# Kernel tuning notes

Hardware: AMD Instinct MI355X
Metric: run time of the kernel (lower is better)

The kernel has to match this reference:

```python
import jax, jax.numpy as jnp
import numpy as np
from jax import lax

# dims: B=2, C=dim=64, H=W=128 -> N=16384 tokens; d_inner=128, d_state=16, dt_rank=4, d_conv=4

def setup_inputs() -> dict:
    key = jax.random.key(0)
    ks = jax.random.split(key, 8)
    def n(k, shp, scale=0.02):
        return jax.random.normal(k, shp, jnp.float32) * scale
    d_inner, d_state, dt_rank = 128, 16, 4
    return {
        "x": jax.random.normal(ks[0], (2, 64, 128, 128), jnp.float32),
        "ln_w": jnp.ones((64,), jnp.float32),
        "ln_b": jnp.zeros((64,), jnp.float32),
        "in_proj_w": n(ks[1], (2 * d_inner, 64)),
        "conv_w": n(ks[2], (d_inner, 1, 4), 0.1),
        "conv_b": jnp.zeros((d_inner,), jnp.float32),
        "x_proj_w": n(ks[3], (dt_rank + 2 * d_state, d_inner)),
        "dt_proj_w": n(ks[4], (d_inner, dt_rank), 0.5),
        "dt_proj_b": n(ks[5], (d_inner,), 0.1),
        "A_log": jnp.log(jnp.broadcast_to(jnp.arange(1, d_state + 1, dtype=jnp.float32), (d_inner, d_state))),
        "D_param": jnp.ones((d_inner,), jnp.float32),
        "out_proj_w": n(ks[6], (64, d_inner)),
        "out_proj_b": jnp.zeros((64,), jnp.float32),
    }


def reference(x, ln_w, ln_b, in_proj_w, conv_w, conv_b, x_proj_w,
              dt_proj_w, dt_proj_b, A_log, D_param, out_proj_w, out_proj_b):
    B, C, H, W = x.shape
    d_inner = in_proj_w.shape[0] // 2
    d_state = A_log.shape[1]
    dt_rank = dt_proj_w.shape[1]
    eps = 1e-5

    # feature2token + channel LayerNorm (Restormer WithBias LN over C)
    t = x.reshape(B, C, H * W).transpose(0, 2, 1)  # [B, N, C]
    mu = jnp.mean(t, axis=-1, keepdims=True)
    var = jnp.var(t, axis=-1, keepdims=True)
    t = (t - mu) * lax.rsqrt(var + eps) * ln_w + ln_b

    # in_proj -> x, z
    xz = jnp.einsum('bnc,dc->bnd', t, in_proj_w)  # [B, N, 2*d_inner]
    x_in, z = jnp.split(xz, 2, axis=-1)

    # depthwise causal conv1d (k=4, pad left 3), then SiLU
    u = lax.conv_general_dilated(
        x_in.transpose(0, 2, 1), conv_w,
        window_strides=(1,), padding=[(3, 0)],
        feature_group_count=d_inner,
        dimension_numbers=('NCH', 'OIH', 'NCH'))
    u = jax.nn.silu(u + conv_b[None, :, None]).transpose(0, 2, 1)  # [B, N, d_inner]

    # x_proj -> dt, B, C of the SSM
    x_dbl = jnp.einsum('bnd,ed->bne', u, x_proj_w)
    dt_r = x_dbl[..., :dt_rank]
    Bmat = x_dbl[..., dt_rank:dt_rank + d_state]   # [B, N, d_state]
    Cmat = x_dbl[..., dt_rank + d_state:]          # [B, N, d_state]
    dt = jax.nn.softplus(jnp.einsum('bnr,dr->bnd', dt_r, dt_proj_w) + dt_proj_b)

    # selective scan: h_t = exp(dt*A) h_{t-1} + dt*B*u
    A = -jnp.exp(A_log)  # [d_inner, d_state]
    deltaA = jnp.exp(jnp.einsum('bnd,ds->bnds', dt, A))
    deltaBu = jnp.einsum('bnd,bns,bnd->bnds', dt, Bmat, u)

    def combine(c1, c2):
        a1, b1 = c1
        a2, b2 = c2
        return a2 * a1, a2 * b1 + b2

    _, h = lax.associative_scan(combine, (deltaA, deltaBu), axis=1)  # h: [B, N, d_inner, d_state]

    y = jnp.einsum('bnds,bns->bnd', h, Cmat) + u * D_param
    y = y * jax.nn.silu(z)
    out = jnp.einsum('bnd,cd->bnc', y, out_proj_w) + out_proj_b  # [B, N, C]

    # token2feature
    return out.transpose(0, 2, 1).reshape(B, C, H, W)
```

## Files before the change

### kernel.cpp

```cpp
#include <hip/hip_runtime.h>
#include <math.h>

#define NTOK 16384
#define DIN  128
#define NCH  512
#define CHL  32
#define NG   16

__device__ __forceinline__ float silu_f(float x)    { return x / (1.f + __expf(-x)); }
__device__ __forceinline__ float softplus_f(float x){ return (x > 20.f) ? x : log1pf(__expf(x)); }

__global__ __launch_bounds__(256) void k1_ln_inproj(
    const float* __restrict__ x, const float* __restrict__ lnw,
    const float* __restrict__ lnb, const float* __restrict__ Win,
    float* __restrict__ xin, float* __restrict__ zbuf)
{
  __shared__ __align__(16) float tl[64*68];
  __shared__ __align__(16) float wt[64*132];
  __shared__ float ps[256], pq[256], mu[64], rs[64];

  int t = threadIdx.x;
  int lane = t & 63, grp = t >> 6;
  int b  = blockIdx.x >> 8;
  int n0 = (blockIdx.x & 255) << 6;
  const float* xb = x + ((size_t)b * 64) * NTOK;

  for (int i = 0; i < 16; ++i) {
    int c = grp*16 + i;
    tl[c*68 + lane] = xb[(size_t)c*NTOK + n0 + lane];
  }
  __syncthreads();
  float s0 = 0.f, s1 = 0.f;
  for (int i = 0; i < 16; ++i) {
    float v = tl[(grp*16+i)*68 + lane];
    s0 += v; s1 += v*v;
  }
  ps[t] = s0; pq[t] = s1;
  __syncthreads();
  if (t < 64) {
    float m = ps[t] + ps[64+t] + ps[128+t] + ps[192+t];
    float q = pq[t] + pq[64+t] + pq[128+t] + pq[192+t];
    m *= 0.015625f;
    q = q*0.015625f - m*m;
    mu[t] = m; rs[t] = rsqrtf(q + 1e-5f);
  }
  __syncthreads();
  for (int i = 0; i < 16; ++i) {
    int idx = (i<<8) + t;
    int c = idx >> 6, j = idx & 63;
    tl[c*68 + j] = (tl[c*68 + j] - mu[j]) * rs[j] * lnw[c] + lnb[c];
  }

  int dl = t & 127, drow = t >> 7;
  int d0 = (lane & 31) << 2;
  int joff = grp*8 + ((lane >> 5) << 2);
  for (int half = 0; half < 2; ++half) {
    __syncthreads();
    for (int i = 0; i < 32; ++i) {
      int c = drow*32 + i;
      wt[c*132 + dl] = Win[((half<<7) + dl)*64 + c];
    }
    __syncthreads();
    for (int p = 0; p < 2; ++p) {
      int jb = joff + (p << 5);
      float acc[4][4] = {{0.f}};
      #pragma unroll 8
      for (int c = 0; c < 64; ++c) {
        float4 tv = *(const float4*)&tl[c*68 + jb];
        float4 wv = *(const float4*)&wt[c*132 + d0];
        acc[0][0] += tv.x*wv.x; acc[0][1] += tv.x*wv.y; acc[0][2] += tv.x*wv.z; acc[0][3] += tv.x*wv.w;
        acc[1][0] += tv.y*wv.x; acc[1][1] += tv.y*wv.y; acc[1][2] += tv.y*wv.z; acc[1][3] += tv.y*wv.w;
        acc[2][0] += tv.z*wv.x; acc[2][1] += tv.z*wv.y; acc[2][2] += tv.z*wv.z; acc[2][3] += tv.z*wv.w;
        acc[3][0] += tv.w*wv.x; acc[3][1] += tv.w*wv.y; acc[3][2] += tv.w*wv.z; acc[3][3] += tv.w*wv.w;
      }
      #pragma unroll
      for (int jj = 0; jj < 4; ++jj) {
        long n = (long)b*NTOK + n0 + jb + jj;
        float4 o = make_float4(acc[jj][0], acc[jj][1], acc[jj][2], acc[jj][3]);
        if (half == 0) {
          *(float4*)&xin[n*128 + d0] = o;
        } else {
          o.x = silu_f(o.x); o.y = silu_f(o.y); o.z = silu_f(o.z); o.w = silu_f(o.w);
          *(float4*)&zbuf[n*128 + d0] = o;
        }
      }
    }
  }
}

__global__ __launch_bounds__(256) void k2_conv(
    const float* __restrict__ xin, const float* __restrict__ cw,
    const float* __restrict__ cb, float* __restrict__ u)
{
  int t = threadIdx.x;
  int d = t & 127;
  long g = (long)blockIdx.x*2 + (t >> 7);
  int n  = (int)(g & (NTOK-1));
  float acc = cb[d];
  #pragma unroll
  for (int k = 0; k < 4; ++k) {
    int m = n - 3 + k;
    if (m >= 0) acc += cw[d*4 + k] * xin[(g - 3 + k)*128 + d];
  }
  u[g*128 + d] = silu_f(acc);
}

__global__ __launch_bounds__(256) void k3_xproj_dt(
    const float* __restrict__ u, const float* __restrict__ Wx,
    const float* __restrict__ Wdt, const float* __restrict__ db,
    float* __restrict__ dt, float* __restrict__ Bm, float* __restrict__ Cm)
{
  __shared__ __align__(16) float wx[36*128];
  __shared__ float wdtT[4*128];
  __shared__ __align__(16) float xdbl[64*40];
  int t = threadIdx.x;
  for (int i = t; i < 1152; i += 256)
    *(float4*)&wx[i*4] = *(const float4*)&Wx[i*4];
  for (int i = t; i < 512; i += 256)
    wdtT[(i&3)*128 + (i>>2)] = Wdt[i];
  __syncthreads();

  long tok0 = (long)blockIdx.x * 64;
  int tok = t & 63, grp = t >> 6;
  const float* urow = u + (tok0 + tok)*128;

  float acc[9];
  #pragma unroll
  for (int e = 0; e < 9; ++e) acc[e] = 0.f;
  #pragma unroll 8
  for (int d4 = 0; d4 < 32; ++d4) {
    float4 uv = *(const float4*)&urow[d4*4];
    #pragma unroll
    for (int e = 0; e < 9; ++e) {
      float4 wv = *(const float4*)&wx[(grp*9+e)*128 + d4*4];
      acc[e] += uv.x*wv.x + uv.y*wv.y + uv.z*wv.z + uv.w*wv.w;
    }
  }
  #pragma unroll
  for (int e = 0; e < 9; ++e) xdbl[tok*40 + grp*9 + e] = acc[e];
  __syncthreads();

  {
    int tk = t >> 2, q = t & 3;
    float4 bv = *(const float4*)&xdbl[tk*40 + 4  + q*4];
    float4 cv = *(const float4*)&xdbl[tk*40 + 20 + q*4];
    *(float4*)&Bm[(tok0+tk)*16 + q*4] = bv;
    *(float4*)&Cm[(tok0+tk)*16 + q*4] = cv;
  }
  int d = t & 127, th = t >> 7;
  float w0 = wdtT[d], w1 = wdtT[128+d], w2 = wdtT[256+d], w3 = wdtT[384+d];
  float bias = db[d];
  for (int j = 0; j < 32; ++j) {
    int tk = th*32 + j;
    float a = bias + xdbl[tk*40]*w0 + xdbl[tk*40+1]*w1
                   + xdbl[tk*40+2]*w2 + xdbl[tk*40+3]*w3;
    dt[(tok0+tk)*128 + d] = softplus_f(a);
  }
}

__global__ __launch_bounds__(128) void k4a_local(
    const float* __restrict__ dt, const float* __restrict__ u,
    const float* __restrict__ Bm, const float* __restrict__ Alog,
    float* __restrict__ carP, float* __restrict__ carH)
{
  int d = threadIdx.x;
  int b = blockIdx.x / NCH, ch = blockIdx.x % NCH;
  long nb = (long)b*NTOK + (long)ch*CHL;
  float A[16], h[16], P[16];
  #pragma unroll
  for (int k = 0; k < 4; ++k) {
    float4 a = *(const float4*)&Alog[d*16 + k*4];
    A[k*4+0] = -__expf(a.x); A[k*4+1] = -__expf(a.y);
    A[k*4+2] = -__expf(a.z); A[k*4+3] = -__expf(a.w);
  }
  #pragma unroll
  for (int s = 0; s < 16; ++s) { h[s] = 0.f; P[s] = 1.f; }
  for (int i = 0; i < CHL; ++i) {
    long n = nb + i;
    float dtv = dt[n*128 + d];
    float uv  = u [n*128 + d];
    float du  = dtv * uv;
    float Bv[16];
    #pragma unroll
    for (int k = 0; k < 4; ++k) {
      float4 v = *(const float4*)&Bm[n*16 + k*4];
      Bv[k*4]=v.x; Bv[k*4+1]=v.y; Bv[k*4+2]=v.z; Bv[k*4+3]=v.w;
    }
    #pragma unroll
    for (int s = 0; s < 16; ++s) {
      float dA = __expf(dtv * A[s]);
      h[s] = dA*h[s] + du*Bv[s];
      P[s] *= dA;
    }
  }
  long cbs = ((long)(b*NCH + ch)*128 + d) * 16;
  #pragma unroll
  for (int k = 0; k < 4; ++k) {
    *(float4*)&carP[cbs + k*4] = make_float4(P[k*4],P[k*4+1],P[k*4+2],P[k*4+3]);
    *(float4*)&carH[cbs + k*4] = make_float4(h[k*4],h[k*4+1],h[k*4+2],h[k*4+3]);
  }
}

__global__ __launch_bounds__(256) void k4b1_group(
    float* __restrict__ cP, float* __restrict__ cH,
    float* __restrict__ Pg, float* __restrict__ Hg)
{
  int idx = blockIdx.x*256 + threadIdx.x;
  int rem = idx & 2047;
  int g   = (idx >> 11) & (NG-1);
  int b   = idx >> 15;
  float P = 1.f, H = 0.f;
  long base = ((long)b*NCH + g*32)*2048 + rem;
  for (int j = 0; j < 32; ++j) {
    long a = base + (long)j*2048;
    float p = cP[a], h = cH[a];
    cP[a] = P; cH[a] = H;
    H = p*H + h;
    P = p*P;
  }
  long ga = ((long)b*NG + g)*2048 + rem;
  Pg[ga] = P; Hg[ga] = H;
}

__global__ __launch_bounds__(256) void k4b2_carry(
    const float* __restrict__ Pg, float* __restrict__ Hg)
{
  int idx = blockIdx.x*256 + threadIdx.x;
  int b = idx >> 11, rem = idx & 2047;
  float H = 0.f;
  for (int g = 0; g < NG; ++g) {
    long a = ((long)b*NG + g)*2048 + rem;
    float p = Pg[a], h = Hg[a];
    Hg[a] = H;
    H = p*H + h;
  }
}

__global__ __launch_bounds__(128) void k4c_apply(
    const float* __restrict__ dt, const float* __restrict__ u,
    const float* __restrict__ Bm, const float* __restrict__ Cm,
    const float* __restrict__ Alog, const float* __restrict__ Dp,
    const float* __restrict__ zs, const float* __restrict__ pPre,
    const float* __restrict__ hPre, const float* __restrict__ Hg,
    float* __restrict__ yz)
{
  int d = threadIdx.x;
  int b = blockIdx.x / NCH, ch = blockIdx.x % NCH;
  long nb = (long)b*NTOK + (long)ch*CHL;
  float A[16], h[16];
  #pragma unroll
  for (int k = 0; k < 4; ++k) {
    float4 a = *(const float4*)&Alog[d*16 + k*4];
    A[k*4+0] = -__expf(a.x); A[k*4+1] = -__expf(a.y);
    A[k*4+2] = -__expf(a.z); A[k*4+3] = -__expf(a.w);
  }
  long cbs = ((long)(b*NCH + ch)*128 + d) * 16;
  long gbs = ((long)b*NG + (ch >> 5))*2048 + d*16;
  #pragma unroll
  for (int k = 0; k < 4; ++k) {
    float4 hp = *(const float4*)&hPre[cbs + k*4];
    float4 pp = *(const float4*)&pPre[cbs + k*4];
    float4 gi = *(const float4*)&Hg[gbs + k*4];
    h[k*4+0] = hp.x + pp.x*gi.x; h[k*4+1] = hp.y + pp.y*gi.y;
    h[k*4+2] = hp.z + pp.z*gi.z; h[k*4+3] = hp.w + pp.w*gi.w;
  }
  float Dv = Dp[d];
  for (int i = 0; i < CHL; ++i) {
    long n = nb + i;
    float dtv = dt[n*128 + d];
    float uv  = u [n*128 + d];
    float du  = dtv * uv;
    float Bv[16], Cv[16];
    #pragma unroll
    for (int k = 0; k < 4; ++k) {
      float4 v = *(const float4*)&Bm[n*16 + k*4];
      Bv[k*4]=v.x; Bv[k*4+1]=v.y; Bv[k*4+2]=v.z; Bv[k*4+3]=v.w;
      float4 w = *(const float4*)&Cm[n*16 + k*4];
      Cv[k*4]=w.x; Cv[k*4+1]=w.y; Cv[k*4+2]=w.z; Cv[k*4+3]=w.w;
    }
    float y = 0.f;
    #pragma unroll
    for (int s = 0; s < 16; ++s) {
      float dA = __expf(dtv * A[s]);
      h[s] = dA*h[s] + du*Bv[s];
      y += h[s]*Cv[s];
    }
    y = (y + uv*Dv) * zs[n*128 + d];
    yz[n*128 + d] = y;
  }
}

__global__ __launch_bounds__(256) void k6_outproj(
    const float* __restrict__ yz, const float* __restrict__ Wout,
    const float* __restrict__ ob, float* __restrict__ out)
{
  __shared__ __align__(16) float wo[64*132];
  __shared__ __align__(16) float yl[32*132];
  int t = threadIdx.x;
  long tok0 = (long)blockIdx.x * 32;
  for (int i = 0; i < 8; ++i) {
    int g = i*256 + t; int c = g >> 5, q = g & 31;
    *(float4*)&wo[c*132 + q*4] = *(const float4*)&Wout[c*128 + q*4];
  }
  for (int i = 0; i < 4; ++i) {
    int g = i*256 + t; int tok = g >> 5, q = g & 31;
    *(float4*)&yl[tok*132 + q*4] = *(const float4*)&yz[(tok0 + tok)*128 + q*4];
  }
  __syncthreads();
  int tp = t & 15;
  int tg = t >> 4;
  float acc[4][2] = {{0.f}};
  for (int d4 = 0; d4 < 32; ++d4) {
    float4 y0 = *(const float4*)&yl[tg*132 + d4*4];
    float4 y1 = *(const float4*)&yl[(tg+16)*132 + d4*4];
    #pragma unroll
    for (int cc = 0; cc < 4; ++cc) {
      float4 wv = *(const float4*)&wo[(tp + 16*cc)*132 + d4*4];
      acc[cc][0] += wv.x*y0.x + wv.y*y0.y + wv.z*y0.z + wv.w*y0.w;
      acc[cc][1] += wv.x*y1.x + wv.y*y1.y + wv.z*y1.z + wv.w*y1.w;
    }
  }
  int b  = (int)(tok0 / NTOK);
  long n0 = tok0 % NTOK;
  #pragma unroll
  for (int cc = 0; cc < 4; ++cc) {
    int c = tp + 16*cc;
    float bias = ob[c];
    out[((long)b*64 + c)*NTOK + n0 + tg     ] = acc[cc][0] + bias;
    out[((long)b*64 + c)*NTOK + n0 + tg + 16] = acc[cc][1] + bias;
  }
}

extern "C" void kernel_launch(void* const* d_in, const int* in_sizes, int n_in,
                              void* d_out, int out_size, void* d_ws, size_t ws_size,
                              hipStream_t stream)
{
  (void)in_sizes; (void)n_in; (void)out_size; (void)ws_size;
  const float* x    = (const float*)d_in[0];
  const float* lnw  = (const float*)d_in[1];
  const float* lnb  = (const float*)d_in[2];
  const float* Win  = (const float*)d_in[3];
  const float* cw   = (const float*)d_in[4];
  const float* cb   = (const float*)d_in[5];
  const float* Wx   = (const float*)d_in[6];
  const float* Wdt  = (const float*)d_in[7];
  const float* db   = (const float*)d_in[8];
  const float* Alog = (const float*)d_in[9];
  const float* Dp   = (const float*)d_in[10];
  const float* Wout = (const float*)d_in[11];
  const float* ob   = (const float*)d_in[12];
  float* out = (float*)d_out;

  float* w   = (float*)d_ws;
  float* xin = w;
  float* z   = w + 4194304;
  float* u   = w + 8388608;
  float* dt  = w + 12582912;
  float* Bm  = w + 16777216;
  float* Cm  = w + 17301504;
  float* cP  = w + 17825792;
  float* cH  = w + 19922944;
  float* Pg  = w + 22020096;
  float* Hg  = w + 22085632;

  k1_ln_inproj<<<512,  256, 0, stream>>>(x, lnw, lnb, Win, xin, z);
  k2_conv     <<<16384,256, 0, stream>>>(xin, cw, cb, u);
  k3_xproj_dt <<<512,  256, 0, stream>>>(u, Wx, Wdt, db, dt, Bm, Cm);
  k4a_local   <<<1024, 128, 0, stream>>>(dt, u, Bm, Alog, cP, cH);
  k4b1_group  <<<256,  256, 0, stream>>>(cP, cH, Pg, Hg);
  k4b2_carry  <<<16,   256, 0, stream>>>(Pg, Hg);
  k4c_apply   <<<1024, 128, 0, stream>>>(dt, u, Bm, Cm, Alog, Dp, z, cP, cH, Hg, xin);
  k6_outproj  <<<1024, 256, 0, stream>>>(xin, Wout, ob, out);
}
```

Measured before the change: 164.4 us.

## Fuse conv, x_proj/dt and local chunk scan into one kernel; rebalance carry groups

Merges the depthwise conv+SiLU, the x_proj/dt_proj computation and the per-chunk local scan into a single kernel. u stays in registers and swizzled shared memory, and B comes from shared memory, so u, dt and Bm are no longer re-read from global memory and two launches disappear. The carry stage now uses 32 groups of 16 chunks instead of 16 of 32, which gives the group kernel twice as many threads and a shorter serial loop. The fused kernel uses more shared memory (an extra 32KB tile) and only 512 blocks, which may reduce occupancy and parallelism compared with the separate 1024-block scan.

```diff
diff --git a/kernel.cpp b/kernel.cpp
--- a/kernel.cpp
+++ b/kernel.cpp
@@ -5,7 +5,8 @@
 #define DIN  128
 #define NCH  512
 #define CHL  32
-#define NG   16
+#define NG   32
+#define GCH  16
 
 __device__ __forceinline__ float silu_f(float x)    { return x / (1.f + __expf(-x)); }
 __device__ __forceinline__ float softplus_f(float x){ return (x > 20.f) ? x : log1pf(__expf(x)); }
@@ -88,84 +89,78 @@
   }
 }
 
-__global__ __launch_bounds__(256) void k2_conv(
+__global__ __launch_bounds__(256) void k23a(
     const float* __restrict__ xin, const float* __restrict__ cw,
-    const float* __restrict__ cb, float* __restrict__ u)
-{
-  int t = threadIdx.x;
-  int d = t & 127;
-  long g = (long)blockIdx.x*2 + (t >> 7);
-  int n  = (int)(g & (NTOK-1));
-  float acc = cb[d];
-  #pragma unroll
-  for (int k = 0; k < 4; ++k) {
-    int m = n - 3 + k;
-    if (m >= 0) acc += cw[d*4 + k] * xin[(g - 3 + k)*128 + d];
-  }
-  u[g*128 + d] = silu_f(acc);
-}
-
-__global__ __launch_bounds__(256) void k3_xproj_dt(
-    const float* __restrict__ u, const float* __restrict__ Wx,
+    const float* __restrict__ cb, const float* __restrict__ Wx,
     const float* __restrict__ Wdt, const float* __restrict__ db,
-    float* __restrict__ dt, float* __restrict__ Bm, float* __restrict__ Cm)
+    const float* __restrict__ Alog,
+    float* __restrict__ u, float* __restrict__ dt,
+    float* __restrict__ Bm, float* __restrict__ Cm,
+    float* __restrict__ carP, float* __restrict__ carH)
 {
   __shared__ __align__(16) float wx[36*128];
   __shared__ float wdtT[4*128];
   __shared__ __align__(16) float xdbl[64*40];
+  __shared__ __align__(16) float ul[64*128];
+
   int t = threadIdx.x;
   for (int i = t; i < 1152; i += 256)
     *(float4*)&wx[i*4] = *(const float4*)&Wx[i*4];
   for (int i = t; i < 512; i += 256)
     wdtT[(i&3)*128 + (i>>2)] = Wdt[i];
-  __syncthreads();
-
-  long tok0 = (long)blockIdx.x * 64;
-  int tok = t & 63, grp = t >> 6;
-  const float* urow = u + (tok0 + tok)*128;
-
-  float acc[9];
-  #pragma unroll
-  for (int e = 0; e < 9; ++e) acc[e] = 0.f;
-  #pragma unroll 8
-  for (int d4 = 0; d4 < 32; ++d4) {
-    float4 uv = *(const float4*)&urow[d4*4];
-    #pragma unroll
-    for (int e = 0; e < 9; ++e) {
-      float4 wv = *(const float4*)&wx[(grp*9+e)*128 + d4*4];
-      acc[e] += uv.x*wv.x + uv.y*wv.y + uv.z*wv.z + uv.w*wv.w;
-    }
-  }
-  #pragma unroll
-  for (int e = 0; e < 9; ++e) xdbl[tok*40 + grp*9 + e] = acc[e];
+
+  int d  = t & 127, th = t >> 7;
+  int b  = blockIdx.x >> 8;
+  int n0 = (blockIdx.x & 255) << 6;
+  int nb0 = n0 + th*32;
+  long g0 = (long)b*NTOK + nb0;
+
+  float w0 = cw[d*4], w1 = cw[d*4+1], w2 = cw[d*4+2], w3 = cw[d*4+3];
+  float cbv = cb[d];
+  float xa = (nb0 >= 3) ? xin[(g0-3)*128 + d] : 0.f;
+  float xb2= (nb0 >= 2) ? xin[(g0-2)*128 + d] : 0.f;
+  float xc = (nb0 >= 1) ? xin[(g0-1)*128 + d] : 0.f;
+  float ureg[32];
+  #pragma unroll
+  for (int j = 0; j < 32; ++j) {
+    float xd = xin[(g0+j)*128 + d];
+    float uv = silu_f(w0*xa + w1*xb2 + w2*xc + w3*xd + cbv);
+    ureg[j] = uv;
+    int nt = th*32 + j;
+    ul[nt*128 + (((d>>2) ^ (nt&31))<<2) + (d&3)] = uv;
+    u[(g0+j)*128 + d] = uv;
+    xa = xb2; xb2 = xc; xc = xd;
+  }
+  __syncthreads();
+
+  {
+    int tok = t & 63, grp = t >> 6;
+    float acc[9];
+    #pragma unroll
+    for (int e = 0; e < 9; ++e) acc[e] = 0.f;
+    #pragma unroll 8
+    for (int d4 = 0; d4 < 32; ++d4) {
+      float4 uv = *(const float4*)&ul[tok*128 + ((d4 ^ (tok&31))<<2)];
+      #pragma unroll
+      for (int e = 0; e < 9; ++e) {
+        float4 wv = *(const float4*)&wx[(grp*9+e)*128 + d4*4];
+        acc[e] += uv.x*wv.x + uv.y*wv.y + uv.z*wv.z + uv.w*wv.w;
+      }
+    }
+    #pragma unroll
+    for (int e = 0; e < 9; ++e) xdbl[tok*40 + grp*9 + e] = acc[e];
+  }
   __syncthreads();
 
   {
     int tk = t >> 2, q = t & 3;
-    float4 bv = *(const float4*)&xdbl[tk*40 + 4  + q*4];
-    float4 cv = *(const float4*)&xdbl[tk*40 + 20 + q*4];
-    *(float4*)&Bm[(tok0+tk)*16 + q*4] = bv;
-    *(float4*)&Cm[(tok0+tk)*16 + q*4] = cv;
-  }
-  int d = t & 127, th = t >> 7;
-  float w0 = wdtT[d], w1 = wdtT[128+d], w2 = wdtT[256+d], w3 = wdtT[384+d];
+    long tok = (long)b*NTOK + n0 + tk;
+    *(float4*)&Bm[tok*16 + q*4] = *(const float4*)&xdbl[tk*40 + 4  + q*4];
+    *(float4*)&Cm[tok*16 + q*4] = *(const float4*)&xdbl[tk*40 + 20 + q*4];
+  }
+
+  float wd0 = wdtT[d], wd1 = wdtT[128+d], wd2 = wdtT[256+d], wd3 = wdtT[384+d];
   float bias = db[d];
-  for (int j = 0; j < 32; ++j) {
-    int tk = th*32 + j;
-    float a = bias + xdbl[tk*40]*w0 + xdbl[tk*40+1]*w1
-                   + xdbl[tk*40+2]*w2 + xdbl[tk*40+3]*w3;
-    dt[(tok0+tk)*128 + d] = softplus_f(a);
-  }
-}
-
-__global__ __launch_bounds__(128) void k4a_local(
-    const float* __restrict__ dt, const float* __restrict__ u,
-    const float* __restrict__ Bm, const float* __restrict__ Alog,
-    float* __restrict__ carP, float* __restrict__ carH)
-{
-  int d = threadIdx.x;
-  int b = blockIdx.x / NCH, ch = blockIdx.x % NCH;
-  long nb = (long)b*NTOK + (long)ch*CHL;
   float A[16], h[16], P[16];
   #pragma unroll
   for (int k = 0; k < 4; ++k) {
@@ -175,15 +170,18 @@
   }
   #pragma unroll
   for (int s = 0; s < 16; ++s) { h[s] = 0.f; P[s] = 1.f; }
-  for (int i = 0; i < CHL; ++i) {
-    long n = nb + i;
-    float dtv = dt[n*128 + d];
-    float uv  = u [n*128 + d];
-    float du  = dtv * uv;
+  #pragma unroll
+  for (int j = 0; j < 32; ++j) {
+    int nt = th*32 + j;
+    float a = bias + xdbl[nt*40]*wd0 + xdbl[nt*40+1]*wd1
+                   + xdbl[nt*40+2]*wd2 + xdbl[nt*40+3]*wd3;
+    float dtv = softplus_f(a);
+    dt[(g0+j)*128 + d] = dtv;
+    float du = dtv * ureg[j];
     float Bv[16];
     #pragma unroll
     for (int k = 0; k < 4; ++k) {
-      float4 v = *(const float4*)&Bm[n*16 + k*4];
+      float4 v = *(const float4*)&xdbl[nt*40 + 4 + k*4];
       Bv[k*4]=v.x; Bv[k*4+1]=v.y; Bv[k*4+2]=v.z; Bv[k*4+3]=v.w;
     }
     #pragma unroll
@@ -193,7 +191,8 @@
       P[s] *= dA;
     }
   }
-  long cbs = ((long)(b*NCH + ch)*128 + d) * 16;
+  int chb = (blockIdx.x & 255)*2 + th;
+  long cbs = ((long)(b*NCH + chb)*128 + d) * 16;
   #pragma unroll
   for (int k = 0; k < 4; ++k) {
     *(float4*)&carP[cbs + k*4] = make_float4(P[k*4],P[k*4+1],P[k*4+2],P[k*4+3]);
@@ -208,10 +207,11 @@
   int idx = blockIdx.x*256 + threadIdx.x;
   int rem = idx & 2047;
   int g   = (idx >> 11) & (NG-1);
-  int b   = idx >> 15;
+  int b   = idx >> 16;
   float P = 1.f, H = 0.f;
-  long base = ((long)b*NCH + g*32)*2048 + rem;
-  for (int j = 0; j < 32; ++j) {
+  long base = ((long)b*NCH + g*GCH)*2048 + rem;
+  #pragma unroll 4
+  for (int j = 0; j < GCH; ++j) {
     long a = base + (long)j*2048;
     float p = cP[a], h = cH[a];
     cP[a] = P; cH[a] = H;
@@ -228,6 +228,7 @@
   int idx = blockIdx.x*256 + threadIdx.x;
   int b = idx >> 11, rem = idx & 2047;
   float H = 0.f;
+  #pragma unroll 4
   for (int g = 0; g < NG; ++g) {
     long a = ((long)b*NG + g)*2048 + rem;
     float p = Pg[a], h = Hg[a];
@@ -255,7 +256,7 @@
     A[k*4+2] = -__expf(a.z); A[k*4+3] = -__expf(a.w);
   }
   long cbs = ((long)(b*NCH + ch)*128 + d) * 16;
-  long gbs = ((long)b*NG + (ch >> 5))*2048 + d*16;
+  long gbs = ((long)b*NG + (ch >> 4))*2048 + d*16;
   #pragma unroll
   for (int k = 0; k < 4; ++k) {
     float4 hp = *(const float4*)&hPre[cbs + k*4];
@@ -361,14 +362,13 @@
   float* cP  = w + 17825792;
   float* cH  = w + 19922944;
   float* Pg  = w + 22020096;
-  float* Hg  = w + 22085632;
-
-  k1_ln_inproj<<<512,  256, 0, stream>>>(x, lnw, lnb, Win, xin, z);
-  k2_conv     <<<16384,256, 0, stream>>>(xin, cw, cb, u);
-  k3_xproj_dt <<<512,  256, 0, stream>>>(u, Wx, Wdt, db, dt, Bm, Cm);
-  k4a_local   <<<1024, 128, 0, stream>>>(dt, u, Bm, Alog, cP, cH);
-  k4b1_group  <<<256,  256, 0, stream>>>(cP, cH, Pg, Hg);
-  k4b2_carry  <<<16,   256, 0, stream>>>(Pg, Hg);
-  k4c_apply   <<<1024, 128, 0, stream>>>(dt, u, Bm, Cm, Alog, Dp, z, cP, cH, Hg, xin);
-  k6_outproj  <<<1024, 256, 0, stream>>>(xin, Wout, ob, out);
-}
+  float* Hg  = w + 22151168;
+
+  k1_ln_inproj<<<512, 256, 0, stream>>>(x, lnw, lnb, Win, xin, z);
+  k23a        <<<512, 256, 0, stream>>>(xin, cw, cb, Wx, Wdt, db, Alog,
+                                        u, dt, Bm, Cm, cP, cH);
+  k4b1_group  <<<512, 256, 0, stream>>>(cP, cH, Pg, Hg);
+  k4b2_carry  <<<16,  256, 0, stream>>>(Pg, Hg);
+  k4c_apply   <<<1024,128, 0, stream>>>(dt, u, Bm, Cm, Alog, Dp, z, cP, cH, Hg, xin);
+  k6_outproj  <<<1024,256, 0, stream>>>(xin, Wout, ob, out);
+}
```

Result: slower. 215.8 us (+31.2%).
